# Optimization experiments

Hardware: AMD Instinct MI355X
Metric: run time of the kernel (lower is better)

The kernel has to match this reference:

```python
import jax, jax.numpy as jnp
import numpy as np

B, C, H, W = 4, 256, 64, 64
D, K = 256, 32
EPS = 1e-12  # F.normalize clamp

def setup_inputs() -> dict:
    key = jax.random.key(0)
    k1, k2, k3, k4 = jax.random.split(key, 4)
    x = jax.random.normal(k1, (B, C, H, W), dtype=jnp.float32)
    w_theta = jax.random.normal(k2, (D, C), dtype=jnp.float32) * 0.05  # 1x1 conv theta
    w_phi = jax.random.normal(k3, (K, C // K), dtype=jnp.float32) * 0.1  # grouped 1x1 conv phi
    scale = jax.random.uniform(k4, (D, K), dtype=jnp.float32, minval=-1.0, maxval=0.0)
    return {"x": x, "w_theta": w_theta, "w_phi": w_phi, "scale": scale}

def reference(x, w_theta, w_phi, scale):
    b, c, h, w = x.shape
    d, k = scale.shape
    n = h * w
    xf = x.reshape(b, c, n)                                   # B,D,N (C==D)
    # --- Gen_code ---
    xg = xf.reshape(b, k, c // k, n)                          # grouped 1x1 conv
    x_phi = jnp.einsum('bkcn,kc->bnk', xg, w_phi)             # B,N,K
    x_phi = jax.nn.softmax(x_phi, axis=1)                     # softmax over pixels
    x_theta = jnp.einsum('dc,bcn->bdn', w_theta, xf)          # B,D,N
    code = jnp.einsum('bdn,bnk->bdk', x_theta, x_phi)         # B,D,K
    code = code / jnp.maximum(jnp.linalg.norm(code, axis=1, keepdims=True), EPS)
    # (dropout p=0.15 treated as identity)
    # --- embedded residual, without materializing B,N,D,K ---
    s2 = scale * scale                                        # D,K
    t1 = jnp.einsum('bdn,dk->bnk', xf * xf, s2)
    t2 = jnp.einsum('bdn,bdk->bnk', xf, s2[None] * code)
    t3 = jnp.einsum('dk,bdk->bk', s2, code * code)
    dist = t1 - 2.0 * t2 + t3[:, None, :]                     # sum_d (scale*(x-code))^2
    Q = jax.nn.softmax(-0.5 * dist, axis=2)                   # B,N,K
    Qsum = Q.sum(axis=1)                                      # B,K
    # Z_[b,d,k] = sum_n Q*residual / Qsum = scale*(sum_n Q x / Qsum - code)
    Z_ = scale[None] * (jnp.einsum('bdn,bnk->bdk', xf, Q) / Qsum[:, None, :] - code)
    Z = Z_ / jnp.sqrt((Z_ * Z_).sum(axis=1, keepdims=True))   # torch sqrt, no eps
    return Z, Q
```

## Files before the change

### kernel.cpp

```cpp
#include <hip/hip_runtime.h>
#include <math.h>

#define BB 4
#define CC 256
#define NN 4096
#define KK 32
#define DD 256
#define GG 8
#define NT2 64
#define NE 8
#define NSL 64

__device__ __forceinline__ float wredsum(float v) {
#pragma unroll
  for (int o = 32; o > 0; o >>= 1) v += __shfl_xor(v, o, 64);
  return v;
}

__global__ __launch_bounds__(256) void k_phi(const float* __restrict__ x,
                                             const float* __restrict__ wphi,
                                             float* __restrict__ phi,
                                             float* __restrict__ SpE) {
  const int b = blockIdx.x >> 6;
  const int sl = blockIdx.x & 63;
  const int n0 = sl * 64;
  const int tid = threadIdx.x;
  __shared__ float phis[64 * 33];
  __shared__ float sred[8 * 33];
  {
    const int kk = tid >> 3;
    const int m = tid & 7;
    const float* xb = x + (size_t)(b * CC + kk * GG) * NN + n0 + m * 8;
    float w[GG];
#pragma unroll
    for (int j = 0; j < GG; ++j) w[j] = wphi[kk * GG + j];
    float4 s0 = make_float4(0.f, 0.f, 0.f, 0.f);
    float4 s1 = make_float4(0.f, 0.f, 0.f, 0.f);
#pragma unroll
    for (int j = 0; j < GG; ++j) {
      const float4 xa = *reinterpret_cast<const float4*>(xb + (size_t)j * NN);
      const float4 xc = *reinterpret_cast<const float4*>(xb + (size_t)j * NN + 4);
      s0.x = fmaf(xa.x, w[j], s0.x);
      s0.y = fmaf(xa.y, w[j], s0.y);
      s0.z = fmaf(xa.z, w[j], s0.z);
      s0.w = fmaf(xa.w, w[j], s0.w);
      s1.x = fmaf(xc.x, w[j], s1.x);
      s1.y = fmaf(xc.y, w[j], s1.y);
      s1.z = fmaf(xc.z, w[j], s1.z);
      s1.w = fmaf(xc.w, w[j], s1.w);
    }
    const int nb = m * 8;
    phis[(nb + 0) * 33 + kk] = __expf(s0.x);
    phis[(nb + 1) * 33 + kk] = __expf(s0.y);
    phis[(nb + 2) * 33 + kk] = __expf(s0.z);
    phis[(nb + 3) * 33 + kk] = __expf(s0.w);
    phis[(nb + 4) * 33 + kk] = __expf(s1.x);
    phis[(nb + 5) * 33 + kk] = __expf(s1.y);
    phis[(nb + 6) * 33 + kk] = __expf(s1.z);
    phis[(nb + 7) * 33 + kk] = __expf(s1.w);
  }
  __syncthreads();
  {
    const int k = tid & 31;
    const int g = tid >> 5;
    float s = 0.f;
#pragma unroll
    for (int i = 0; i < 8; ++i) s += phis[(g * 8 + i) * 33 + k];
    sred[g * 33 + k] = s;
  }
  __syncthreads();
  {
    const int n = tid >> 2;
    const int k0 = (tid & 3) * 8;
    float v[8];
#pragma unroll
    for (int j = 0; j < 8; ++j) v[j] = phis[n * 33 + k0 + j];
    float* dst = phi + ((size_t)b * NN + n0 + n) * KK + k0;
    float4 o0 = make_float4(v[0], v[1], v[2], v[3]);
    float4 o1 = make_float4(v[4], v[5], v[6], v[7]);
    *reinterpret_cast<float4*>(dst + 0) = o0;
    *reinterpret_cast<float4*>(dst + 4) = o1;
    if (tid < 32) {
      float s = 0.f;
#pragma unroll
      for (int g = 0; g < 8; ++g) s += sred[g * 33 + tid];
      SpE[((size_t)sl * BB + b) * KK + tid] = s;
    }
  }
}

__global__ __launch_bounds__(256) void k_xp(const float* __restrict__ x,
                                            const float* __restrict__ p,
                                            float* __restrict__ outq) {
  const int e = blockIdx.x & 7;
  const int ct = (blockIdx.x >> 3) & 31;
  const int b = blockIdx.x >> 8;
  const int tid = threadIdx.x;
  const int k = tid & 31;
  const int g = tid >> 5;
  const int n0 = e * 512 + g * 64;
  const float* xb = x + (size_t)(b * CC + ct * 8) * NN;
  const float* pb = p + (size_t)b * NN * KK + k;
  float acc[8] = {0.f, 0.f, 0.f, 0.f, 0.f, 0.f, 0.f, 0.f};
  for (int n = n0; n < n0 + 64; n += 4) {
    const float p0 = pb[(size_t)(n + 0) * KK];
    const float p1 = pb[(size_t)(n + 1) * KK];
    const float p2 = pb[(size_t)(n + 2) * KK];
    const float p3 = pb[(size_t)(n + 3) * KK];
#pragma unroll
    for (int c = 0; c < 8; ++c) {
      const float4 xv = *reinterpret_cast<const float4*>(xb + (size_t)c * NN + n);
      acc[c] = fmaf(xv.x, p0, acc[c]);
      acc[c] = fmaf(xv.y, p1, acc[c]);
      acc[c] = fmaf(xv.z, p2, acc[c]);
      acc[c] = fmaf(xv.w, p3, acc[c]);
    }
  }
  __shared__ float lds[8 * 8 * 33];
#pragma unroll
  for (int c = 0; c < 8; ++c) lds[(g * 8 + c) * 33 + k] = acc[c];
  __syncthreads();
  const int c2 = tid & 7, k2 = tid >> 3;
  float s = 0.f;
#pragma unroll
  for (int gg = 0; gg < 8; ++gg) s += lds[(gg * 8 + c2) * 33 + k2];
  outq[((size_t)(e * BB + b) * KK + k2) * CC + ct * 8 + c2] = s;
}

__global__ __launch_bounds__(256) void k_code(const float* __restrict__ m1e,
                                              const float* __restrict__ SpE,
                                              const float* __restrict__ wth,
                                              const float* __restrict__ scale,
                                              float* __restrict__ code,
                                              float* __restrict__ bc2,
                                              float* __restrict__ s2g,
                                              float* __restrict__ t3) {
  const int b = blockIdx.x >> 5;
  const int k = blockIdx.x & 31;
  const int d = threadIdx.x;
  __shared__ __align__(16) float m1s[CC];
  __shared__ float rb[4];
  float sp = (d < NSL) ? SpE[((size_t)d * BB + b) * KK + k] : 0.f;
  sp = wredsum(sp);
  if ((d & 63) == 0) rb[d >> 6] = sp;
  __syncthreads();
  const float invS = 1.f / (rb[0] + rb[1] + rb[2] + rb[3]);
  float m = 0.f;
#pragma unroll
  for (int e = 0; e < NE; ++e)
    m += m1e[((size_t)(e * BB + b) * KK + k) * CC + d];
  m1s[d] = m * invS;
  __syncthreads();
  float c0 = 0.f, c1 = 0.f, c2 = 0.f, c3 = 0.f;
  const float* wt = wth + (size_t)d * CC;
#pragma unroll 4
  for (int c = 0; c < CC; c += 4) {
    const float4 w4 = *reinterpret_cast<const float4*>(wt + c);
    const float4 m4 = *reinterpret_cast<const float4*>(&m1s[c]);
    c0 = fmaf(w4.x, m4.x, c0);
    c1 = fmaf(w4.y, m4.y, c1);
    c2 = fmaf(w4.z, m4.z, c2);
    c3 = fmaf(w4.w, m4.w, c3);
  }
  float cd = (c0 + c1) + (c2 + c3);
  float ss = wredsum(cd * cd);
  __syncthreads();
  if ((d & 63) == 0) rb[d >> 6] = ss;
  __syncthreads();
  const float nrm = sqrtf(rb[0] + rb[1] + rb[2] + rb[3]);
  const float inv = 1.f / fmaxf(nrm, 1e-12f);
  cd *= inv;
  const float sc = scale[(size_t)d * KK + k];
  const float s2 = sc * sc;
  code[((size_t)b * DD + d) * KK + k] = cd;
  bc2[((size_t)b * DD + d) * KK + k] = 2.f * s2 * cd;
  if (b == 0) s2g[(size_t)d * KK + k] = s2;
  float tt = wredsum(s2 * cd * cd);
  __syncthreads();
  if ((d & 63) == 0) rb[d >> 6] = tt;
  __syncthreads();
  if (d == 0) t3[b * KK + k] = rb[0] + rb[1] + rb[2] + rb[3];
}

__global__ __launch_bounds__(512) void k_dist(const float* __restrict__ x,
                                              const float* __restrict__ s2g,
                                              const float* __restrict__ bc2,
                                              const float* __restrict__ t3,
                                              float* __restrict__ qout,
                                              float* __restrict__ qpart) {
  const int b = blockIdx.x >> 6;
  const int tile = blockIdx.x & 63;
  const int n0 = tile * 64;
  const int tid = threadIdx.x;
  const int lane = tid & 63;
  const int wid = __builtin_amdgcn_readfirstlane(tid >> 6);
  const int d0 = wid * 32;
  __shared__ float lds[4 * 64 * 33];
  __shared__ float smax[64 * 9];
  __shared__ float ssum[64 * 9];
  float accA[32], accB[32];
#pragma unroll
  for (int k = 0; k < 32; ++k) { accA[k] = 0.f; accB[k] = 0.f; }
  const float* xb = x + ((size_t)b * CC + d0) * NN + n0 + lane;
  const float* s2b = s2g + (size_t)d0 * KK;
  const float* bcb = bc2 + ((size_t)b * DD + d0) * KK;
#pragma unroll 2
  for (int dd = 0; dd < 32; ++dd) {
    const float xv = xb[(size_t)dd * NN];
    const float x2 = xv * xv;
    const float* s2r = s2b + dd * KK;
    const float* bcr = bcb + dd * KK;
#pragma unroll
    for (int k = 0; k < 32; ++k) {
      accA[k] = fmaf(x2, s2r[k], accA[k]);
      accB[k] = fmaf(xv, bcr[k], accB[k]);
    }
  }
  if (wid >= 4) {
    float* Lp = lds + ((size_t)((wid - 4) * 64 + lane)) * 33;
#pragma unroll
    for (int k = 0; k < 32; ++k) Lp[k] = accA[k] - accB[k];
  }
  __syncthreads();
  if (wid < 4) {
    float* Lp = lds + ((size_t)(wid * 64 + lane)) * 33;
#pragma unroll
    for (int k = 0; k < 32; ++k) Lp[k] += accA[k] - accB[k];
  }
  __syncthreads();
  const int n = lane;
  const int kq = wid;
  float vals[4];
#pragma unroll
  for (int j = 0; j < 4; ++j) {
    const int k = kq * 4 + j;
    float s = 0.f;
#pragma unroll
    for (int g = 0; g < 4; ++g) s += lds[((size_t)(g * 64 + n)) * 33 + k];
    vals[j] = -0.5f * (s + t3[b * KK + k]);
  }
  float m4 = fmaxf(fmaxf(vals[0], vals[1]), fmaxf(vals[2], vals[3]));
  smax[n * 9 + kq] = m4;
  __syncthreads();
  float m = smax[n * 9 + 0];
#pragma unroll
  for (int g = 1; g < 8; ++g) m = fmaxf(m, smax[n * 9 + g]);
  float e[4];
  float ps = 0.f;
#pragma unroll
  for (int j = 0; j < 4; ++j) {
    e[j] = __expf(vals[j] - m);
    ps += e[j];
  }
  ssum[n * 9 + kq] = ps;
  __syncthreads();
  float tot = 0.f;
#pragma unroll
  for (int g = 0; g < 8; ++g) tot += ssum[n * 9 + g];
  const float inv = 1.f / tot;
  float4 q4;
  q4.x = e[0] * inv; q4.y = e[1] * inv;
  q4.z = e[2] * inv; q4.w = e[3] * inv;
  *reinterpret_cast<float4*>(qout + ((size_t)b * NN + n0 + n) * KK + kq * 4) =
      q4;
  float qs[4] = {q4.x, q4.y, q4.z, q4.w};
#pragma unroll
  for (int j = 0; j < 4; ++j) {
    const float v = wredsum(qs[j]);
    if (n == 0) qpart[((size_t)b * KK + kq * 4 + j) * NT2 + tile] = v;
  }
}

__global__ __launch_bounds__(256) void k_z(const float* __restrict__ znq8,
                                           const float* __restrict__ code,
                                           const float* __restrict__ scale,
                                           const float* __restrict__ qpart,
                                           float* __restrict__ zout) {
  const int b = blockIdx.x >> 5;
  const int k = blockIdx.x & 31;
  const int d = threadIdx.x;
  __shared__ float rb[4];
  float qp = (d < NT2) ? qpart[((size_t)b * KK + k) * NT2 + d] : 0.f;
  qp = wredsum(qp);
  if ((d & 63) == 0) rb[d >> 6] = qp;
  __syncthreads();
  const float qs = rb[0] + rb[1] + rb[2] + rb[3];
  float zn = 0.f;
#pragma unroll
  for (int e = 0; e < NE; ++e)
    zn += znq8[((size_t)(e * BB + b) * KK + k) * CC + d];
  const float cd = code[((size_t)b * DD + d) * KK + k];
  const float z_ = scale[(size_t)d * KK + k] * (zn / qs - cd);
  float ss = wredsum(z_ * z_);
  __syncthreads();
  if ((d & 63) == 0) rb[d >> 6] = ss;
  __syncthreads();
  const float rn = 1.f / sqrtf(rb[0] + rb[1] + rb[2] + rb[3]);
  zout[((size_t)b * DD + d) * KK + k] = z_ * rn;
}

extern "C" void kernel_launch(void* const* d_in, const int* in_sizes, int n_in,
                              void* d_out, int out_size, void* d_ws,
                              size_t ws_size, hipStream_t stream) {
  const float* x = (const float*)d_in[0];
  const float* wth = (const float*)d_in[1];
  const float* wphi = (const float*)d_in[2];
  const float* scale = (const float*)d_in[3];
  float* out = (float*)d_out;
  float* zout = out;
  float* qout = out + (size_t)BB * DD * KK;
  float* ws = (float*)d_ws;
  float* phi = ws;
  float* SpE = phi + (size_t)BB * NN * KK;
  float* m1e = SpE + (size_t)NSL * BB * KK;
  float* code = m1e + (size_t)NE * BB * KK * CC;
  float* bc2 = code + (size_t)BB * DD * KK;
  float* s2g = bc2 + (size_t)BB * DD * KK;
  float* t3 = s2g + (size_t)DD * KK;
  float* qpart = t3 + BB * KK;
  float* znq8 = qpart + (size_t)BB * KK * NT2;

  k_phi<<<BB * NSL, 256, 0, stream>>>(x, wphi, phi, SpE);
  k_xp<<<BB * 32 * NE, 256, 0, stream>>>(x, phi, m1e);
  k_code<<<BB * KK, 256, 0, stream>>>(m1e, SpE, wth, scale, code, bc2, s2g, t3);
  k_dist<<<BB * NT2, 512, 0, stream>>>(x, s2g, bc2, t3, qout, qpart);
  k_xp<<<BB * 32 * NE, 256, 0, stream>>>(x, qout, znq8);
  k_z<<<BB * KK, 256, 0, stream>>>(znq8, code, scale, qpart, zout);
}
```

Measured before the change: 78.18 us.

## Fuse phi softmax-exp and x·phi accumulation into one kernel

```diff
diff --git a/kernel.cpp b/kernel.cpp
--- a/kernel.cpp
+++ b/kernel.cpp
@@ -17,16 +17,16 @@
   return v;
 }
 
-__global__ __launch_bounds__(256) void k_phi(const float* __restrict__ x,
+__global__ __launch_bounds__(256) void k_pm1(const float* __restrict__ x,
                                              const float* __restrict__ wphi,
-                                             float* __restrict__ phi,
+                                             float* __restrict__ m1e,
                                              float* __restrict__ SpE) {
-  const int b = blockIdx.x >> 6;
-  const int sl = blockIdx.x & 63;
-  const int n0 = sl * 64;
+  const int b = blockIdx.x >> 8;
+  const int ct = (blockIdx.x >> 6) & 3;
+  const int e = blockIdx.x & 63;
+  const int n0 = e * 64;
   const int tid = threadIdx.x;
   __shared__ float phis[64 * 33];
-  __shared__ float sred[8 * 33];
   {
     const int kk = tid >> 3;
     const int m = tid & 7;
@@ -60,32 +60,178 @@
     phis[(nb + 7) * 33 + kk] = __expf(s1.w);
   }
   __syncthreads();
-  {
-    const int k = tid & 31;
-    const int g = tid >> 5;
+  if (ct == 0 && tid < 32) {
     float s = 0.f;
-#pragma unroll
-    for (int i = 0; i < 8; ++i) s += phis[(g * 8 + i) * 33 + k];
-    sred[g * 33 + k] = s;
-  }
-  __syncthreads();
-  {
-    const int n = tid >> 2;
-    const int k0 = (tid & 3) * 8;
-    float v[8];
-#pragma unroll
-    for (int j = 0; j < 8; ++j) v[j] = phis[n * 33 + k0 + j];
-    float* dst = phi + ((size_t)b * NN + n0 + n) * KK + k0;
-    float4 o0 = make_float4(v[0], v[1], v[2], v[3]);
-    float4 o1 = make_float4(v[4], v[5], v[6], v[7]);
-    *reinterpret_cast<float4*>(dst + 0) = o0;
-    *reinterpret_cast<float4*>(dst + 4) = o1;
-    if (tid < 32) {
-      float s = 0.f;
-#pragma unroll
-      for (int g = 0; g < 8; ++g) s += sred[g * 33 + tid];
-      SpE[((size_t)sl * BB + b) * KK + tid] = s;
+#pragma unroll 8
+    for (int n = 0; n < 64; ++n) s += phis[n * 33 + tid];
+    SpE[((size_t)e * BB + b) * KK + tid] = s;
+  }
+  const int k = tid & 31;
+  const int g = tid >> 5;
+  const int c0 = ct * 64 + g * 8;
+  const float* xm = x + (size_t)(b * CC + c0) * NN + n0;
+  float acc[8] = {0.f, 0.f, 0.f, 0.f, 0.f, 0.f, 0.f, 0.f};
+  for (int n = 0; n < 64; n += 4) {
+    const float p0 = phis[(n + 0) * 33 + k];
+    const float p1 = phis[(n + 1) * 33 + k];
+    const float p2 = phis[(n + 2) * 33 + k];
+    const float p3 = phis[(n + 3) * 33 + k];
+#pragma unroll
+    for (int c = 0; c < 8; ++c) {
+      const float4 xv = *reinterpret_cast<const float4*>(xm + (size_t)c * NN + n);
+      acc[c] = fmaf(xv.x, p0, acc[c]);
+      acc[c] = fmaf(xv.y, p1, acc[c]);
+      acc[c] = fmaf(xv.z, p2, acc[c]);
+      acc[c] = fmaf(xv.w, p3, acc[c]);
     }
+  }
+  float* mb = m1e + (((size_t)e * BB + b) * KK + k) * CC + c0;
+  float4 o0 = make_float4(acc[0], acc[1], acc[2], acc[3]);
+  float4 o1 = make_float4(acc[4], acc[5], acc[6], acc[7]);
+  *reinterpret_cast<float4*>(mb + 0) = o0;
+  *reinterpret_cast<float4*>(mb + 4) = o1;
+}
+
+__global__ __launch_bounds__(256) void k_code(const float* __restrict__ m1e,
+                                              const float* __restrict__ SpE,
+                                              const float* __restrict__ wth,
+                                              const float* __restrict__ scale,
+                                              float* __restrict__ code,
+                                              float* __restrict__ bc2,
+                                              float* __restrict__ s2g,
+                                              float* __restrict__ t3) {
+  const int b = blockIdx.x >> 5;
+  const int k = blockIdx.x & 31;
+  const int d = threadIdx.x;
+  __shared__ __align__(16) float m1s[CC];
+  __shared__ float rb[4];
+  float sp = (d < NSL) ? SpE[((size_t)d * BB + b) * KK + k] : 0.f;
+  sp = wredsum(sp);
+  if ((d & 63) == 0) rb[d >> 6] = sp;
+  __syncthreads();
+  const float invS = 1.f / (rb[0] + rb[1] + rb[2] + rb[3]);
+  float m = 0.f;
+  for (int e = 0; e < NSL; ++e)
+    m += m1e[(((size_t)e * BB + b) * KK + k) * CC + d];
+  m1s[d] = m * invS;
+  __syncthreads();
+  float c0 = 0.f, c1 = 0.f, c2 = 0.f, c3 = 0.f;
+  const float* wt = wth + (size_t)d * CC;
+#pragma unroll 4
+  for (int c = 0; c < CC; c += 4) {
+    const float4 w4 = *reinterpret_cast<const float4*>(wt + c);
+    const float4 m4 = *reinterpret_cast<const float4*>(&m1s[c]);
+    c0 = fmaf(w4.x, m4.x, c0);
+    c1 = fmaf(w4.y, m4.y, c1);
+    c2 = fmaf(w4.z, m4.z, c2);
+    c3 = fmaf(w4.w, m4.w, c3);
+  }
+  float cd = (c0 + c1) + (c2 + c3);
+  float ss = wredsum(cd * cd);
+  __syncthreads();
+  if ((d & 63) == 0) rb[d >> 6] = ss;
+  __syncthreads();
+  const float nrm = sqrtf(rb[0] + rb[1] + rb[2] + rb[3]);
+  const float inv = 1.f / fmaxf(nrm, 1e-12f);
+  cd *= inv;
+  const float sc = scale[(size_t)d * KK + k];
+  const float s2 = sc * sc;
+  code[((size_t)b * DD + d) * KK + k] = cd;
+  bc2[((size_t)b * DD + d) * KK + k] = 2.f * s2 * cd;
+  if (b == 0) s2g[(size_t)d * KK + k] = s2;
+  float tt = wredsum(s2 * cd * cd);
+  __syncthreads();
+  if ((d & 63) == 0) rb[d >> 6] = tt;
+  __syncthreads();
+  if (d == 0) t3[b * KK + k] = rb[0] + rb[1] + rb[2] + rb[3];
+}
+
+__global__ __launch_bounds__(512) void k_dist(const float* __restrict__ x,
+                                              const float* __restrict__ s2g,
+                                              const float* __restrict__ bc2,
+                                              const float* __restrict__ t3,
+                                              float* __restrict__ qout,
+                                              float* __restrict__ qpart) {
+  const int b = blockIdx.x >> 6;
+  const int tile = blockIdx.x & 63;
+  const int n0 = tile * 64;
+  const int tid = threadIdx.x;
+  const int lane = tid & 63;
+  const int wid = __builtin_amdgcn_readfirstlane(tid >> 6);
+  const int d0 = wid * 32;
+  __shared__ float lds[4 * 64 * 33];
+  __shared__ float smax[64 * 9];
+  __shared__ float ssum[64 * 9];
+  float accA[32], accB[32];
+#pragma unroll
+  for (int k = 0; k < 32; ++k) { accA[k] = 0.f; accB[k] = 0.f; }
+  const float* xb = x + ((size_t)b * CC + d0) * NN + n0 + lane;
+  const float* s2b = s2g + (size_t)d0 * KK;
+  const float* bcb = bc2 + ((size_t)b * DD + d0) * KK;
+#pragma unroll 2
+  for (int dd = 0; dd < 32; ++dd) {
+    const float xv = xb[(size_t)dd * NN];
+    const float x2 = xv * xv;
+    const float* s2r = s2b + dd * KK;
+    const float* bcr = bcb + dd * KK;
+#pragma unroll
+    for (int k = 0; k < 32; ++k) {
+      accA[k] = fmaf(x2, s2r[k], accA[k]);
+      accB[k] = fmaf(xv, bcr[k], accB[k]);
+    }
+  }
+  if (wid >= 4) {
+    float* Lp = lds + ((size_t)((wid - 4) * 64 + lane)) * 33;
+#pragma unroll
+    for (int k = 0; k < 32; ++k) Lp[k] = accA[k] - accB[k];
+  }
+  __syncthreads();
+  if (wid < 4) {
+    float* Lp = lds + ((size_t)(wid * 64 + lane)) * 33;
+#pragma unroll
+    for (int k = 0; k < 32; ++k) Lp[k] += accA[k] - accB[k];
+  }
+  __syncthreads();
+  const int n = lane;
+  const int kq = wid;
+  float vals[4];
+#pragma unroll
+  for (int j = 0; j < 4; ++j) {
+    const int k = kq * 4 + j;
+    float s = 0.f;
+#pragma unroll
+    for (int g = 0; g < 4; ++g) s += lds[((size_t)(g * 64 + n)) * 33 + k];
+    vals[j] = -0.5f * (s + t3[b * KK + k]);
+  }
+  float m4 = fmaxf(fmaxf(vals[0], vals[1]), fmaxf(vals[2], vals[3]));
+  smax[n * 9 + kq] = m4;
+  __syncthreads();
+  float m = smax[n * 9 + 0];
+#pragma unroll
+  for (int g = 1; g < 8; ++g) m = fmaxf(m, smax[n * 9 + g]);
+  float e[4];
+  float ps = 0.f;
+#pragma unroll
+  for (int j = 0; j < 4; ++j) {
+    e[j] = __expf(vals[j] - m);
+    ps += e[j];
+  }
+  ssum[n * 9 + kq] = ps;
+  __syncthreads();
+  float tot = 0.f;
+#pragma unroll
+  for (int g = 0; g < 8; ++g) tot += ssum[n * 9 + g];
+  const float inv = 1.f / tot;
+  float4 q4;
+  q4.x = e[0] * inv; q4.y = e[1] * inv;
+  q4.z = e[2] * inv; q4.w = e[3] * inv;
+  *reinterpret_cast<float4*>(qout + ((size_t)b * NN + n0 + n) * KK + kq * 4) =
+      q4;
+  float qs[4] = {q4.x, q4.y, q4.z, q4.w};
+#pragma unroll
+  for (int j = 0; j < 4; ++j) {
+    const float v = wredsum(qs[j]);
+    if (n == 0) qpart[((size_t)b * KK + kq * 4 + j) * NT2 + tile] = v;
   }
 }
 
@@ -127,150 +273,6 @@
   outq[((size_t)(e * BB + b) * KK + k2) * CC + ct * 8 + c2] = s;
 }
 
-__global__ __launch_bounds__(256) void k_code(const float* __restrict__ m1e,
-                                              const float* __restrict__ SpE,
-                                              const float* __restrict__ wth,
-                                              const float* __restrict__ scale,
-                                              float* __restrict__ code,
-                                              float* __restrict__ bc2,
-                                              float* __restrict__ s2g,
-                                              float* __restrict__ t3) {
-  const int b = blockIdx.x >> 5;
-  const int k = blockIdx.x & 31;
-  const int d = threadIdx.x;
-  __shared__ __align__(16) float m1s[CC];
-  __shared__ float rb[4];
-  float sp = (d < NSL) ? SpE[((size_t)d * BB + b) * KK + k] : 0.f;
-  sp = wredsum(sp);
-  if ((d & 63) == 0) rb[d >> 6] = sp;
-  __syncthreads();
-  const float invS = 1.f / (rb[0] + rb[1] + rb[2] + rb[3]);
-  float m = 0.f;
-#pragma unroll
-  for (int e = 0; e < NE; ++e)
-    m += m1e[((size_t)(e * BB + b) * KK + k) * CC + d];
-  m1s[d] = m * invS;
-  __syncthreads();
-  float c0 = 0.f, c1 = 0.f, c2 = 0.f, c3 = 0.f;
-  const float* wt = wth + (size_t)d * CC;
-#pragma unroll 4
-  for (int c = 0; c < CC; c += 4) {
-    const float4 w4 = *reinterpret_cast<const float4*>(wt + c);
-    const float4 m4 = *reinterpret_cast<const float4*>(&m1s[c]);
-    c0 = fmaf(w4.x, m4.x, c0);
-    c1 = fmaf(w4.y, m4.y, c1);
-    c2 = fmaf(w4.z, m4.z, c2);
-    c3 = fmaf(w4.w, m4.w, c3);
-  }
-  float cd = (c0 + c1) + (c2 + c3);
-  float ss = wredsum(cd * cd);
-  __syncthreads();
-  if ((d & 63) == 0) rb[d >> 6] = ss;
-  __syncthreads();
-  const float nrm = sqrtf(rb[0] + rb[1] + rb[2] + rb[3]);
-  const float inv = 1.f / fmaxf(nrm, 1e-12f);
-  cd *= inv;
-  const float sc = scale[(size_t)d * KK + k];
-  const float s2 = sc * sc;
-  code[((size_t)b * DD + d) * KK + k] = cd;
-  bc2[((size_t)b * DD + d) * KK + k] = 2.f * s2 * cd;
-  if (b == 0) s2g[(size_t)d * KK + k] = s2;
-  float tt = wredsum(s2 * cd * cd);
-  __syncthreads();
-  if ((d & 63) == 0) rb[d >> 6] = tt;
-  __syncthreads();
-  if (d == 0) t3[b * KK + k] = rb[0] + rb[1] + rb[2] + rb[3];
-}
-
-__global__ __launch_bounds__(512) void k_dist(const float* __restrict__ x,
-                                              const float* __restrict__ s2g,
-                                              const float* __restrict__ bc2,
-                                              const float* __restrict__ t3,
-                                              float* __restrict__ qout,
-                                              float* __restrict__ qpart) {
-  const int b = blockIdx.x >> 6;
-  const int tile = blockIdx.x & 63;
-  const int n0 = tile * 64;
-  const int tid = threadIdx.x;
-  const int lane = tid & 63;
-  const int wid = __builtin_amdgcn_readfirstlane(tid >> 6);
-  const int d0 = wid * 32;
-  __shared__ float lds[4 * 64 * 33];
-  __shared__ float smax[64 * 9];
-  __shared__ float ssum[64 * 9];
-  float accA[32], accB[32];
-#pragma unroll
-  for (int k = 0; k < 32; ++k) { accA[k] = 0.f; accB[k] = 0.f; }
-  const float* xb = x + ((size_t)b * CC + d0) * NN + n0 + lane;
-  const float* s2b = s2g + (size_t)d0 * KK;
-  const float* bcb = bc2 + ((size_t)b * DD + d0) * KK;
-#pragma unroll 2
-  for (int dd = 0; dd < 32; ++dd) {
-    const float xv = xb[(size_t)dd * NN];
-    const float x2 = xv * xv;
-    const float* s2r = s2b + dd * KK;
-    const float* bcr = bcb + dd * KK;
-#pragma unroll
-    for (int k = 0; k < 32; ++k) {
-      accA[k] = fmaf(x2, s2r[k], accA[k]);
-      accB[k] = fmaf(xv, bcr[k], accB[k]);
-    }
-  }
-  if (wid >= 4) {
-    float* Lp = lds + ((size_t)((wid - 4) * 64 + lane)) * 33;
-#pragma unroll
-    for (int k = 0; k < 32; ++k) Lp[k] = accA[k] - accB[k];
-  }
-  __syncthreads();
-  if (wid < 4) {
-    float* Lp = lds + ((size_t)(wid * 64 + lane)) * 33;
-#pragma unroll
-    for (int k = 0; k < 32; ++k) Lp[k] += accA[k] - accB[k];
-  }
-  __syncthreads();
-  const int n = lane;
-  const int kq = wid;
-  float vals[4];
-#pragma unroll
-  for (int j = 0; j < 4; ++j) {
-    const int k = kq * 4 + j;
-    float s = 0.f;
-#pragma unroll
-    for (int g = 0; g < 4; ++g) s += lds[((size_t)(g * 64 + n)) * 33 + k];
-    vals[j] = -0.5f * (s + t3[b * KK + k]);
-  }
-  float m4 = fmaxf(fmaxf(vals[0], vals[1]), fmaxf(vals[2], vals[3]));
-  smax[n * 9 + kq] = m4;
-  __syncthreads();
-  float m = smax[n * 9 + 0];
-#pragma unroll
-  for (int g = 1; g < 8; ++g) m = fmaxf(m, smax[n * 9 + g]);
-  float e[4];
-  float ps = 0.f;
-#pragma unroll
-  for (int j = 0; j < 4; ++j) {
-    e[j] = __expf(vals[j] - m);
-    ps += e[j];
-  }
-  ssum[n * 9 + kq] = ps;
-  __syncthreads();
-  float tot = 0.f;
-#pragma unroll
-  for (int g = 0; g < 8; ++g) tot += ssum[n * 9 + g];
-  const float inv = 1.f / tot;
-  float4 q4;
-  q4.x = e[0] * inv; q4.y = e[1] * inv;
-  q4.z = e[2] * inv; q4.w = e[3] * inv;
-  *reinterpret_cast<float4*>(qout + ((size_t)b * NN + n0 + n) * KK + kq * 4) =
-      q4;
-  float qs[4] = {q4.x, q4.y, q4.z, q4.w};
-#pragma unroll
-  for (int j = 0; j < 4; ++j) {
-    const float v = wredsum(qs[j]);
-    if (n == 0) qpart[((size_t)b * KK + kq * 4 + j) * NT2 + tile] = v;
-  }
-}
-
 __global__ __launch_bounds__(256) void k_z(const float* __restrict__ znq8,
                                            const float* __restrict__ code,
                                            const float* __restrict__ scale,
@@ -310,18 +312,16 @@
   float* zout = out;
   float* qout = out + (size_t)BB * DD * KK;
   float* ws = (float*)d_ws;
-  float* phi = ws;
-  float* SpE = phi + (size_t)BB * NN * KK;
+  float* SpE = ws;
   float* m1e = SpE + (size_t)NSL * BB * KK;
-  float* code = m1e + (size_t)NE * BB * KK * CC;
+  float* code = m1e + (size_t)NSL * BB * KK * CC;
   float* bc2 = code + (size_t)BB * DD * KK;
   float* s2g = bc2 + (size_t)BB * DD * KK;
   float* t3 = s2g + (size_t)DD * KK;
   float* qpart = t3 + BB * KK;
   float* znq8 = qpart + (size_t)BB * KK * NT2;
 
-  k_phi<<<BB * NSL, 256, 0, stream>>>(x, wphi, phi, SpE);
-  k_xp<<<BB * 32 * NE, 256, 0, stream>>>(x, phi, m1e);
+  k_pm1<<<BB * NSL * 4, 256, 0, stream>>>(x, wphi, m1e, SpE);
   k_code<<<BB * KK, 256, 0, stream>>>(m1e, SpE, wth, scale, code, bc2, s2g, t3);
   k_dist<<<BB * NT2, 512, 0, stream>>>(x, s2g, bc2, t3, qout, qpart);
   k_xp<<<BB * 32 * NE, 256, 0, stream>>>(x, qout, znq8);
```

Measured after the change: 76.67 us. About the same (-1.9%).
